# Optimization experiments

Measured on AMD Instinct MI355X. Metric: run time of the kernel, lower is better.

## Reference

```python
import jax, jax.numpy as jnp
from jax import lax
import numpy as np

LEVEL_HW = [(100, 100), (50, 50), (25, 25), (13, 13), (7, 7)]  # P3..P7 for 800x800 input
N, C, A, K, NCONV = 2, 256, 9, 80, 4
PRIOR_PROB = 0.01


def conv3x3(x, w, b):
    # x: (N,C,H,W), w: (O,I,3,3), stride 1, pad 1
    y = lax.conv_general_dilated(x, w, (1, 1), 'SAME',
                                 dimension_numbers=('NCHW', 'OIHW', 'NCHW'))
    return y + b[None, :, None, None]


def permute_to_N_HWA_K(t, k):
    # (N, A*k, H, W) -> (N, H*W*A, k), matching the torch helper
    n, _, h, w = t.shape
    return t.reshape(n, -1, k, h, w).transpose(0, 3, 4, 1, 2).reshape(n, -1, k)


def setup_inputs() -> dict:
    key = jax.random.key(0)
    ks = iter(jax.random.split(key, 64))
    inp = {}
    for i, (h, w) in enumerate(LEVEL_HW):
        inp[f"f{i}"] = jax.random.normal(next(ks), (N, C, h, w), jnp.float32)
    for pre in ("cls", "box"):
        for i in range(NCONV):
            inp[f"{pre}_w{i}"] = 0.01 * jax.random.normal(next(ks), (C, C, 3, 3), jnp.float32)
            inp[f"{pre}_b{i}"] = jnp.zeros((C,), jnp.float32)
    bias_value = -float(np.log((1.0 - PRIOR_PROB) / PRIOR_PROB))
    inp["cls_score_w"] = 0.01 * jax.random.normal(next(ks), (A * K, C, 3, 3), jnp.float32)
    inp["cls_score_b"] = jnp.full((A * K,), bias_value, jnp.float32)
    inp["box_pred_w"] = 0.01 * jax.random.normal(next(ks), (A * 4, C, 3, 3), jnp.float32)
    inp["box_pred_b"] = jnp.zeros((A * 4,), jnp.float32)
    return inp


def reference(f0, f1, f2, f3, f4,
              cls_w0, cls_b0, cls_w1, cls_b1, cls_w2, cls_b2, cls_w3, cls_b3,
              box_w0, box_b0, box_w1, box_b1, box_w2, box_b2, box_w3, box_b3,
              cls_score_w, cls_score_b, box_pred_w, box_pred_b):
    feats = [f0, f1, f2, f3, f4]
    cls_p = [(cls_w0, cls_b0), (cls_w1, cls_b1), (cls_w2, cls_b2), (cls_w3, cls_b3)]
    box_p = [(box_w0, box_b0), (box_w1, box_b1), (box_w2, box_b2), (box_w3, box_b3)]
    logits, boxes = [], []
    for f in feats:
        x = f
        for w, b in cls_p:
            x = jax.nn.relu(conv3x3(x, w, b))
        logits.append(permute_to_N_HWA_K(conv3x3(x, cls_score_w, cls_score_b), K))
        y = f
        for w, b in box_p:
            y = jax.nn.relu(conv3x3(y, w, b))
        boxes.append(permute_to_N_HWA_K(conv3x3(y, box_pred_w, box_pred_b), 4))
    # (N, R, K) and (N, R, 4) with R = sum_l Hl*Wl*A = 120087; concat on last dim
    return jnp.concatenate([jnp.concatenate(logits, 1), jnp.concatenate(boxes, 1)], axis=2)
```

## Files before the change

kernel.cpp:

```cpp
#include <hip/hip_runtime.h>


typedef __attribute__((ext_vector_type(8))) short short8;
typedef __attribute__((ext_vector_type(4))) float floatx4;

#define LVLTOT 14143

__device__ __forceinline__ unsigned short f2bf(float f) {
  unsigned int u = __float_as_uint(f);
  unsigned int r = (u + 0x7fffu + ((u >> 16) & 1u)) >> 16;
  return (unsigned short)r;
}

__device__ __forceinline__ void gload_lds16(const void* g, void* l) {
  __builtin_amdgcn_global_load_lds(
      (const __attribute__((address_space(1))) unsigned int*)g,
      (__attribute__((address_space(3))) unsigned int*)l, 16, 0, 0);
}

struct PrepArgs {
  const float* f[5];
  const float* w[10];
  unsigned short* wdst[10];
  int wblk_off[11];
  int cout[10];
  unsigned short* x0;
  unsigned short* bufA;
  unsigned short* bufB;
};

__global__ __launch_bounds__(256) void prep(PrepArgs A) {
  static const int Ht[5] = {100, 50, 25, 13, 7};
  static const int Wpt[5] = {102, 52, 27, 15, 9};
  static const int LOFFt[5] = {0, 10404, 13108, 13837, 14062};
  __shared__ float ts[32][33];
  const int bid = blockIdx.x;
  const int t = threadIdx.x;

  if (bid < 1090) {
    int sid = bid % 545, n = bid / 545;
    int l, h, wb;
    if (sid < 400)      { l = 0; h = sid >> 2; wb = sid & 3; }
    else if (sid < 500) { l = 1; h = (sid - 400) >> 1; wb = (sid - 400) & 1; }
    else if (sid < 525) { l = 2; h = sid - 500; wb = 0; }
    else if (sid < 538) { l = 3; h = sid - 525; wb = 0; }
    else                { l = 4; h = sid - 538; wb = 0; }
    const float* f = A.f[l];
    int H = Ht[l], W = H, Wp = Wpt[l], loff = LOFFt[l];
    int w0 = wb * 32;
    for (int s = 0; s < 8; s++) {
      int ch0 = s * 32;
      __syncthreads();
#pragma unroll
      for (int r4 = 0; r4 < 4; r4++) {
        int ch = ch0 + (t >> 5) + r4 * 8;
        int px = w0 + (t & 31);
        float v = 0.f;
        if (px < W) v = f[(((size_t)n * 256 + ch) * H + h) * W + px];
        ts[(t >> 5) + r4 * 8][t & 31] = v;
      }
      __syncthreads();
      int pxl = t >> 3, c4 = t & 7;
      if (w0 + pxl < W) {
        unsigned short pk[4];
#pragma unroll
        for (int k = 0; k < 4; k++) pk[k] = f2bf(ts[c4 * 4 + k][pxl]);
        *(unsigned long long*)(A.x0 +
            ((size_t)n * LVLTOT + loff + (size_t)(h + 1) * Wp + (w0 + pxl + 1)) *
                256 + ch0 + c4 * 4) = *(unsigned long long*)pk;
      }
    }
    return;
  }

  if (bid < 3970) {
    int b2 = bid - 1090;
    int tix = 0;
    while (b2 >= A.wblk_off[tix + 1]) tix++;
    int co = b2 - A.wblk_off[tix];
    int ci = t;
    bool valid = co < A.cout[tix];
    const float* w = A.w[tix];
    unsigned short* dst = A.wdst[tix];
    int cb = co >> 6, col = co & 63, chk = ci >> 5, qd = (ci >> 3) & 3, j = ci & 7;
#pragma unroll
    for (int tap = 0; tap < 9; tap++) {
      float v = valid ? w[((size_t)co * 256 + ci) * 9 + tap] : 0.f;
      dst[((((size_t)(cb * 8 + chk) * 9 + tap) * 4 + qd) * 64 + col) * 8 + j] =
          f2bf(v);
    }
    return;
  }

  {
    static const int BCUM[6] = {0, 404, 608, 712, 768, 800};
    int b3 = bid - 3970;
    int plane = b3 / 100;
    int item = (b3 % 100) * 256 + t;
    int pxi = item >> 5, oct = item & 31;
    if (pxi >= 800) return;
    int l = 0;
    while (pxi >= BCUM[l + 1]) l++;
    int j = pxi - BCUM[l];
    int Wp = Wpt[l];
    int r, c;
    if (j < Wp)            { r = 0; c = j; }
    else if (j < 2 * Wp)   { r = Wp - 1; c = j - Wp; }
    else { int k = j - 2 * Wp; r = 1 + (k >> 1); c = (k & 1) ? Wp - 1 : 0; }
    size_t px = (size_t)LOFFt[l] + (size_t)r * Wp + c;
    unsigned short* base = (plane < 4)
                               ? (A.bufA + (size_t)plane * LVLTOT * 256)
                               : (A.bufB + (size_t)(plane - 4) * LVLTOT * 256);
    floatx4 z;
    z[0] = z[1] = z[2] = z[3] = 0.f;
    *(floatx4*)(base + px * 256 + oct * 8) = z;
  }
}

__device__ __forceinline__ void decode_seg(int s, int& l, int& h0, int& w0,
                                           int& H, int& Wp, int& loff) {
  if (s < 350)      { l = 0; int hp = s / 7; w0 = (s - hp * 7) * 16; h0 = hp * 2;
                      H = 100; Wp = 102; loff = 0; }
  else if (s < 450) { l = 1; int r = s - 350; h0 = (r >> 2) * 2; w0 = (r & 3) * 16;
                      H = 50; Wp = 52; loff = 10404; }
  else if (s < 476) { l = 2; int r = s - 450; h0 = (r >> 1) * 2; w0 = (r & 1) * 16;
                      H = 25; Wp = 27; loff = 13108; }
  else if (s < 483) { l = 3; h0 = (s - 476) * 2; w0 = 0; H = 13; Wp = 15;
                      loff = 13837; }
  else              { l = 4; h0 = (s - 483) * 2; w0 = 0; H = 7; Wp = 9;
                      loff = 14062; }
}

#define CONV_XPRE()                                                            \
  int xsrc[9];                                                                 \
  _Pragma("unroll") for (int k = 0; k < 9; k++) {                              \
    int u = k * 256 + t;                                                       \
    int qq = u / 576, rem = u - qq * 576;                                      \
    int sl8 = rem / 72, rm2 = rem - sl8 * 72;                                  \
    int r4 = rm2 / 18, c18 = rm2 - r4 * 18;                                    \
    int sg = sblk * 8 + sl8; if (sg > 486) sg = 486;                           \
    int l_, h0_, w0_, H_, Wp_, lo_;                                            \
    decode_seg(sg, l_, h0_, w0_, H_, Wp_, lo_);                                \
    int prow = h0_ + r4; if (prow > H_ + 1) prow = H_ + 1;                     \
    int pcol = w0_ + c18; if (pcol > Wp_ - 1) pcol = Wp_ - 1;                  \
    xsrc[k] = (lo_ + prow * Wp_ + pcol) * 256 + qq * 8;                        \
  }

#define CONV_MAIN_LOOP(INP, WBLOB, CB)                                         \
  {                                                                            \
    _Pragma("unroll 1") for (int ch = 0; ch < 8; ch++) {                       \
      if (ch) __syncthreads();                                                 \
      const unsigned short* wsrc = (WBLOB) + ((size_t)((CB)*8 + ch)) * 18432;  \
      _Pragma("unroll") for (int i = 0; i < 9; i++)                            \
        gload_lds16(wsrc + i * 2048 + wv * 512 + lane * 8,                     \
                    lds_w + i * 2048 + wv * 512);                              \
      _Pragma("unroll") for (int k = 0; k < 9; k++)                            \
        gload_lds16((INP) + xsrc[k] + ch * 32,                                 \
                    lds_x + (size_t)(k * 256 + wv * 64) * 8);                  \
      __syncthreads();                                                         \
      const short8* xw = (const short8*)lds_w;                                 \
      const short8* xx = (const short8*)lds_x;                                 \
      _Pragma("unroll") for (int tdx = 0; tdx < 3; tdx++) {                    \
        short8 bfr[2][4];                                                      \
        _Pragma("unroll") for (int sb = 0; sb < 2; sb++)                       \
          _Pragma("unroll") for (int r = 0; r < 4; r++)                        \
            bfr[sb][r] =                                                       \
                xx[q * 576 + (wv * 2 + sb) * 72 + r * 18 + tdx + n16];         \
        _Pragma("unroll") for (int tdy = 0; tdy < 3; tdy++) {                  \
          const int tap = tdy * 3 + tdx;                                       \
          _Pragma("unroll") for (int cc = 0; cc < 4; cc++) {                   \
            short8 afr = xw[(tap * 4 + q) * 64 + cc * 16 + n16];               \
            _Pragma("unroll") for (int rg = 0; rg < 4; rg++)                   \
              acc[cc][rg] = __builtin_amdgcn_mfma_f32_16x16x32_bf16(           \
                  afr, bfr[rg >> 1][(rg & 1) + tdy], acc[cc][rg], 0, 0, 0);    \
          }                                                                    \
        }                                                                      \
      }                                                                        \
    }                                                                          \
  }

__global__ __launch_bounds__(256, 2) void conv_tower_mfma(
    const unsigned short* __restrict__ xin, unsigned short* __restrict__ xout,
    const unsigned short* __restrict__ wblob_cls,
    const unsigned short* __restrict__ wblob_box,
    const float* __restrict__ bias_cls, const float* __restrict__ bias_box,
    int in_n_stride, int in_tw_stride) {
  const int p = blockIdx.x;
  const int xcd = p & 7, jj = p >> 3;
  const int cnt = (xcd < 4) ? 31 : 30;
  if (jj >= 4 * cnt) return;
  const int tlw = jj >> 2, cb = jj & 3;
  const int tl = tlw * 8 + xcd;
  const int sblk = tl % 61;
  const int zpl = tl / 61;
  const int n = zpl >> 1, tw = zpl & 1;

  __shared__ __align__(16) unsigned short lds_w[18432];
  __shared__ __align__(16) unsigned short lds_x[18432];
  const int t = threadIdx.x, lane = t & 63, wv = t >> 6;
  const int q = lane >> 4, n16 = lane & 15;
  const unsigned short* wblob = tw ? wblob_box : wblob_cls;
  const float* bias = tw ? bias_box : bias_cls;
  const unsigned short* inp =
      xin + ((size_t)n * in_n_stride + (size_t)tw * in_tw_stride) * 256;
  unsigned short* outp = xout + ((size_t)(n * 2 + tw) * LVLTOT) * 256;

  floatx4 acc[4][4];
#pragma unroll
  for (int i = 0; i < 4; i++)
#pragma unroll
    for (int jx = 0; jx < 4; jx++) acc[i][jx] = (floatx4){0.f, 0.f, 0.f, 0.f};

  CONV_XPRE()
  CONV_MAIN_LOOP(inp, wblob, cb)

#pragma unroll
  for (int rg = 0; rg < 4; rg++) {
    int sg = sblk * 8 + wv * 2 + (rg >> 1);
    if (sg > 486) sg = 486;
    int l_, h0_, w0_, H_, Wp_, lo_;
    decode_seg(sg, l_, h0_, w0_, H_, Wp_, lo_);
    int h = h0_ + (rg & 1);
    int w_ = w0_ + n16;
    if (h < H_ && w_ < H_) {
#pragma unroll
      for (int cc = 0; cc < 4; cc++) {
        floatx4 bb = *(const floatx4*)(bias + cb * 64 + cc * 16 + q * 4);
        unsigned short pk[4];
#pragma unroll
        for (int rgi = 0; rgi < 4; rgi++)
          pk[rgi] = f2bf(fmaxf(acc[cc][rg][rgi] + bb[rgi], 0.f));
        size_t base = ((size_t)lo_ + (size_t)(h + 1) * Wp_ + (w_ + 1)) * 256 +
                      cb * 64 + cc * 16 + q * 4;
        *(unsigned long long*)(outp + base) = *(unsigned long long*)pk;
      }
    }
  }
}

__global__ __launch_bounds__(256, 2) void conv_final_mfma(
    const unsigned short* __restrict__ xin, float* __restrict__ out,
    const unsigned short* __restrict__ wblob_cls,
    const unsigned short* __restrict__ wblob_box,
    const float* __restrict__ bias_cls, const float* __restrict__ bias_box) {
  const int p = blockIdx.x;
  const int xcd = p & 7, jj = p >> 3;
  const int cnt = (xcd < 2) ? 16 : 15;
  if (jj >= 13 * cnt) return;
  const int tlw = jj / 13, yb = jj - tlw * 13;
  const int tl = tlw * 8 + xcd;
  const int sblk = tl % 61;
  const int n = tl / 61;

  __shared__ __align__(16) unsigned short lds_w[18432];
  __shared__ __align__(16) unsigned short lds_x[18432];
  const int t = threadIdx.x, lane = t & 63, wv = t >> 6;
  const int q = lane >> 4, n16 = lane & 15;
  const bool is_cls = yb < 12;
  const int cb = is_cls ? yb : 0;
  const int tw = is_cls ? 0 : 1;
  const int Cout = is_cls ? 720 : 36;
  const unsigned short* wblob = is_cls ? wblob_cls : wblob_box;
  const float* bias = is_cls ? bias_cls : bias_box;
  const int RB[5] = {0, 90000, 112500, 118125, 119646};
  const unsigned short* inp = xin + ((size_t)(n * 2 + tw) * LVLTOT) * 256;

  floatx4 acc[4][4];
#pragma unroll
  for (int i = 0; i < 4; i++)
#pragma unroll
    for (int jx = 0; jx < 4; jx++) acc[i][jx] = (floatx4){0.f, 0.f, 0.f, 0.f};

  CONV_XPRE()
  CONV_MAIN_LOOP(inp, wblob, cb)

#pragma unroll
  for (int rg = 0; rg < 4; rg++) {
    int sg = sblk * 8 + wv * 2 + (rg >> 1);
    if (sg > 486) sg = 486;
    int l_, h0_, w0_, H_, Wp_, lo_;
    decode_seg(sg, l_, h0_, w0_, H_, Wp_, lo_);
    int h = h0_ + (rg & 1);
    int w_ = w0_ + n16;
    if (h < H_ && w_ < H_) {
      size_t ridx = (size_t)RB[l_] + ((size_t)h * H_ + w_) * 9;
#pragma unroll
      for (int cc = 0; cc < 4; cc++) {
        int co0 = cb * 64 + cc * 16 + q * 4;
        if (co0 >= Cout) continue;
        floatx4 bb = *(const floatx4*)(bias + co0);
        int a = is_cls ? (co0 / 80) : (co0 >> 2);
        int col0 = is_cls ? (co0 - a * 80) : 80;
        floatx4 v;
#pragma unroll
        for (int rgi = 0; rgi < 4; rgi++) v[rgi] = acc[cc][rg][rgi] + bb[rgi];
        *(floatx4*)(out + ((size_t)n * 120087 + ridx + a) * 84 + col0) = v;
      }
    }
  }
}

extern "C" void kernel_launch(void* const* d_in, const int* in_sizes, int n_in,
                              void* d_out, int out_size, void* d_ws,
                              size_t ws_size, hipStream_t stream) {
  char* ws = (char*)d_ws;
  unsigned short* bufB = (unsigned short*)(ws);
  unsigned short* X0 = (unsigned short*)(ws + 14482432);
  unsigned short* bufA = (unsigned short*)(ws + 28964864);
  unsigned short* tb[8];
  for (int i = 0; i < 8; i++)
    tb[i] = (unsigned short*)(ws + 57929728 + (size_t)i * 1179648);
  unsigned short* fb_cls = (unsigned short*)(ws + 67366912);
  unsigned short* fb_box = (unsigned short*)(ws + 70905856);

  float* out = (float*)d_out;

  PrepArgs pa;
  for (int i = 0; i < 5; i++) pa.f[i] = (const float*)d_in[i];
  for (int i = 0; i < 4; i++) {
    pa.w[i] = (const float*)d_in[5 + 2 * i];
    pa.w[4 + i] = (const float*)d_in[13 + 2 * i];
    pa.wdst[i] = tb[i];
    pa.wdst[4 + i] = tb[4 + i];
    pa.cout[i] = pa.cout[4 + i] = 256;
  }
  pa.w[8] = (const float*)d_in[21]; pa.wdst[8] = fb_cls; pa.cout[8] = 720;
  pa.w[9] = (const float*)d_in[23]; pa.wdst[9] = fb_box; pa.cout[9] = 36;
  int off = 0;
  for (int i = 0; i < 8; i++) { pa.wblk_off[i] = off; off += 256; }
  pa.wblk_off[8] = off; off += 768;
  pa.wblk_off[9] = off; off += 64;
  pa.wblk_off[10] = off;
  pa.x0 = X0;
  pa.bufA = bufA;
  pa.bufB = bufB;

  prep<<<dim3(4770), 256, 0, stream>>>(pa);

  const float *cls_b[4], *box_b[4];
  for (int i = 0; i < 4; i++) {
    cls_b[i] = (const float*)d_in[6 + 2 * i];
    box_b[i] = (const float*)d_in[14 + 2 * i];
  }

  conv_tower_mfma<<<dim3(992), 256, 0, stream>>>(X0, bufA, tb[0], tb[4],
                                                 cls_b[0], box_b[0], LVLTOT, 0);
  conv_tower_mfma<<<dim3(992), 256, 0, stream>>>(
      bufA, bufB, tb[1], tb[5], cls_b[1], box_b[1], 2 * LVLTOT, LVLTOT);
  conv_tower_mfma<<<dim3(992), 256, 0, stream>>>(
      bufB, bufA, tb[2], tb[6], cls_b[2], box_b[2], 2 * LVLTOT, LVLTOT);
  conv_tower_mfma<<<dim3(992), 256, 0, stream>>>(
      bufA, bufB, tb[3], tb[7], cls_b[3], box_b[3], 2 * LVLTOT, LVLTOT);

  conv_final_mfma<<<dim3(1664), 256, 0, stream>>>(
      bufB, out, fb_cls, fb_box, (const float*)d_in[22], (const float*)d_in[24]);
}
```

Baseline: 608.0 us.

## Load conv weight fragments directly from global into registers instead of LDS

Weight tiles were staged through a shared LDS buffer. They are now read straight from global memory into registers, per tap column, and the load for the third column is interleaved with compute on the first. This removes the weight LDS buffer, roughly halving shared memory per block, and cuts LDS read traffic. In exchange every wave reads the weights from global/L2 separately, with no sharing across waves, and register pressure rises (36 short8 registers) under launch_bounds(256,2).

New measurement: 782.7 us. 28.7% more time.

```diff
diff --git a/kernel.cpp b/kernel.cpp
--- a/kernel.cpp
+++ b/kernel.cpp
@@ -146,36 +146,49 @@
     xsrc[k] = (lo_ + prow * Wp_ + pcol) * 256 + qq * 8;                        \
   }
 
+#define WLOAD(DST, XWB, CBASE, TDX)                                            \
+  _Pragma("unroll") for (int u = 0; u < 12; u++) {                             \
+    int tdy_ = u >> 2, cc_ = u & 3;                                            \
+    DST[u] = (XWB)[(CBASE) + (size_t)(((tdy_ * 3 + (TDX)) * 4 + q) * 64 +      \
+                                      cc_ * 16 + n16)];                        \
+  }
+
+#define CONV_TDX(WREG, TDX)                                                    \
+  {                                                                            \
+    short8 bfr[2][4];                                                          \
+    _Pragma("unroll") for (int sb = 0; sb < 2; sb++)                           \
+      _Pragma("unroll") for (int r = 0; r < 4; r++)                            \
+        bfr[sb][r] =                                                           \
+            xx[q * 576 + (wv * 2 + sb) * 72 + r * 18 + (TDX) + n16];           \
+    _Pragma("unroll") for (int tdy = 0; tdy < 3; tdy++) {                      \
+      _Pragma("unroll") for (int cc = 0; cc < 4; cc++) {                       \
+        _Pragma("unroll") for (int rg = 0; rg < 4; rg++)                       \
+          acc[cc][rg] = __builtin_amdgcn_mfma_f32_16x16x32_bf16(               \
+              WREG[tdy * 4 + cc], bfr[rg >> 1][(rg & 1) + tdy], acc[cc][rg],   \
+              0, 0, 0);                                                        \
+      }                                                                        \
+    }                                                                          \
+  }
+
 #define CONV_MAIN_LOOP(INP, WBLOB, CB)                                         \
   {                                                                            \
+    const short8* xwb = (const short8*)(WBLOB);                                \
     _Pragma("unroll 1") for (int ch = 0; ch < 8; ch++) {                       \
       if (ch) __syncthreads();                                                 \
-      const unsigned short* wsrc = (WBLOB) + ((size_t)((CB)*8 + ch)) * 18432;  \
-      _Pragma("unroll") for (int i = 0; i < 9; i++)                            \
-        gload_lds16(wsrc + i * 2048 + wv * 512 + lane * 8,                     \
-                    lds_w + i * 2048 + wv * 512);                              \
       _Pragma("unroll") for (int k = 0; k < 9; k++)                            \
         gload_lds16((INP) + xsrc[k] + ch * 32,                                 \
                     lds_x + (size_t)(k * 256 + wv * 64) * 8);                  \
+      const size_t cbase = (size_t)((CB) * 8 + ch) * 2304;                     \
+      short8 wA[12], wB[12];                                                   \
+      WLOAD(wA, xwb, cbase, 0)                                                 \
+      WLOAD(wB, xwb, cbase, 1)                                                 \
       __syncthreads();                                                         \
-      const short8* xw = (const short8*)lds_w;                                 \
       const short8* xx = (const short8*)lds_x;                                 \
-      _Pragma("unroll") for (int tdx = 0; tdx < 3; tdx++) {                    \
-        short8 bfr[2][4];                                                      \
-        _Pragma("unroll") for (int sb = 0; sb < 2; sb++)                       \
-          _Pragma("unroll") for (int r = 0; r < 4; r++)                        \
-            bfr[sb][r] =                                                       \
-                xx[q * 576 + (wv * 2 + sb) * 72 + r * 18 + tdx + n16];         \
-        _Pragma("unroll") for (int tdy = 0; tdy < 3; tdy++) {                  \
-          const int tap = tdy * 3 + tdx;                                       \
-          _Pragma("unroll") for (int cc = 0; cc < 4; cc++) {                   \
-            short8 afr = xw[(tap * 4 + q) * 64 + cc * 16 + n16];               \
-            _Pragma("unroll") for (int rg = 0; rg < 4; rg++)                   \
-              acc[cc][rg] = __builtin_amdgcn_mfma_f32_16x16x32_bf16(           \
-                  afr, bfr[rg >> 1][(rg & 1) + tdy], acc[cc][rg], 0, 0, 0);    \
-          }                                                                    \
-        }                                                                      \
-      }                                                                        \
+      CONV_TDX(wA, 0)                                                          \
+      short8 wC[12];                                                           \
+      WLOAD(wC, xwb, cbase, 2)                                                 \
+      CONV_TDX(wB, 1)                                                          \
+      CONV_TDX(wC, 2)                                                          \
     }                                                                          \
   }
 
@@ -195,7 +208,6 @@
   const int zpl = tl / 61;
   const int n = zpl >> 1, tw = zpl & 1;
 
-  __shared__ __align__(16) unsigned short lds_w[18432];
   __shared__ __align__(16) unsigned short lds_x[18432];
   const int t = threadIdx.x, lane = t & 63, wv = t >> 6;
   const int q = lane >> 4, n16 = lane & 15;
@@ -252,7 +264,6 @@
   const int sblk = tl % 61;
   const int n = tl / 61;
 
-  __shared__ __align__(16) unsigned short lds_w[18432];
   __shared__ __align__(16) unsigned short lds_x[18432];
   const int t = threadIdx.x, lane = t & 63, wv = t >> 6;
   const int q = lane >> 4, n16 = lane & 15;
```
